# Optimization experiments

Hardware: AMD Instinct MI355X
Metric: run time of the kernel (lower is better)

## Reference

```python
import jax, jax.numpy as jnp
import numpy as np

# Config (matches init_kwargs)
T, B = 128, 32
I, H, O, G = 128, 320, 32, 8
GROUP = 16  # attn_group_size entries, 8 groups of 16 -> sums to I
DT, TAU_X, TAU_W = 0.02, 0.1, 0.2
ALPHA_X = DT / TAU_X          # 0.2
ALPHA_W = DT / TAU_W          # 0.1
E_PROP = 0.8


def _masks():
    e_h = int(E_PROP * H)  # 256
    # x2h: e_prop=1, zero_cols_prop=0, no diag removal -> all ones
    mask_x = jnp.ones((H, I), dtype=jnp.float32)
    # h2h: sign mask (+1 for E, -1 for I), diagonal zeroed
    sign_h = jnp.concatenate([jnp.ones(e_h), -jnp.ones(H - e_h)]).astype(jnp.float32)
    mask_h = jnp.tile(sign_h[None, :], (H, 1)) * (1.0 - jnp.eye(H, dtype=jnp.float32))
    # h2o: zero_cols = int(0.2*H) trailing columns removed, sign mask on the rest
    zc = int((1.0 - E_PROP) * H)  # 64
    exist = jnp.concatenate([jnp.ones(H - zc), jnp.zeros(zc)]).astype(jnp.float32)
    mask_o = jnp.tile((sign_h * exist)[None, :], (O, 1))
    # attn EILinear(H -> G): same column pattern as h2o
    mask_a = jnp.tile((sign_h * exist)[None, :], (G, 1))
    return mask_x, mask_h, mask_o, mask_a


def setup_inputs() -> dict:
    key = jax.random.key(0)
    ks = jax.random.split(key, 10)
    s = 0.05  # keep dynamics in a sane range
    return {
        "x": jax.random.normal(ks[0], (T, B, I), dtype=jnp.float32),
        "Rs": jax.random.uniform(ks[1], (T, B, 1), dtype=jnp.float32),
        "W_x2h": jax.random.normal(ks[2], (H, I), dtype=jnp.float32) * s,
        "W_h2h": jax.random.normal(ks[3], (H, H), dtype=jnp.float32) * s,
        "b_h2h": jax.random.normal(ks[4], (H,), dtype=jnp.float32) * s,
        "W_h2o": jax.random.normal(ks[5], (O, H), dtype=jnp.float32) * s,
        "b_h2o": jax.random.normal(ks[6], (O,), dtype=jnp.float32) * s,
        "W_attn": jax.random.normal(ks[7], (G, H), dtype=jnp.float32) * s,
        "b_attn": jax.random.normal(ks[8], (G,), dtype=jnp.float32) * s,
        "c_plas": jax.random.normal(ks[9], (6,), dtype=jnp.float32) * s,
    }


def reference(x, Rs, W_x2h, W_h2h, b_h2h, W_h2o, b_h2o, W_attn, b_attn, c_plas):
    mask_x, mask_h, mask_o, mask_a = _masks()
    relu = jax.nn.relu
    # effective (sign/existence constrained, positive) weights
    ew_attn = relu(W_attn) * mask_a                      # [G, H]
    ew_x0 = relu(W_x2h) * mask_x                         # [H, I]
    ew_h0 = relu(W_h2h) * mask_h                         # [H, H]
    c = jnp.abs(c_plas)

    state0 = jnp.zeros((B, H), dtype=x.dtype)            # x0=0, sigma_rec=0
    output0 = relu(state0)
    wx0 = jnp.broadcast_to(ew_x0[None], (B, H, I))       # batched fast weights
    wh0 = jnp.broadcast_to(ew_h0[None], (B, H, H))

    def step(carry, inp):
        state, output, wx, wh = carry
        x_t, R_t = inp                                   # [B,I], [B,1]
        # attention over hidden groups
        attn = jax.nn.softmax(output @ ew_attn.T + b_attn, axis=-1)  # [B,G]
        attn_full = jnp.repeat(attn, GROUP, axis=-1)     # [B,I]
        xm = x_t * attn_full * G
        # masked / positive-constrained fast weights applied per batch
        ewx = relu(wx) * mask_x[None]                    # [B,H,I]
        ewh = relu(wh) * mask_h[None]                    # [B,H,H]
        total = (jnp.einsum('bhi,bi->bh', ewx, xm)
                 + jnp.einsum('bhj,bj->bh', ewh, output) + b_h2h)
        new_state = state * (1.0 - ALPHA_X) + total * ALPHA_X
        new_output = jnp.tanh(relu(new_state))           # retanh
        # outer-product plasticity update
        R = R_t[:, :, None]                              # [B,1,1]
        wx_n = wx * (1.0 - ALPHA_W) + ALPHA_W * R * (
            c[0] * xm[:, None, :]
            + c[1] * new_output[:, :, None]
            + c[2] * jnp.einsum('bi,bj->bij', new_output, xm))
        wh_n = wh * (1.0 - ALPHA_W) + ALPHA_W * R * (
            c[3] * output[:, None, :]
            + c[4] * new_output[:, :, None]
            + c[5] * jnp.einsum('bi,bj->bij', new_output, output))
        return (new_state, new_output, wx_n, wh_n), new_output

    _, hs = jax.lax.scan(step, (state0, output0, wx0, wh0), (x, Rs))  # hs: [T,B,H]
    ew_o = relu(W_h2o) * mask_o                          # [O,H]
    out = jax.nn.sigmoid(jnp.einsum('tbh,oh->tbo', hs, ew_o) + b_h2o)
    return out, hs
```

## Files before the change

### kernel.cpp

```cpp
#include <hip/hip_runtime.h>

#define TT 128
#define BB 32
#define II 128
#define HH 320
#define OO 32
#define GG 8
#define HPAD 129

static __device__ __forceinline__ float fexp2(float x) { return __builtin_amdgcn_exp2f(x); }
static __device__ __forceinline__ float frcp(float x)  { return __builtin_amdgcn_rcpf(x); }

static __device__ __forceinline__ float tanh_pos(float x) {
    float e = fexp2(x * 2.8853900817779268f);
    return 1.0f - 2.0f * frcp(e + 1.0f);
}

template<int CTRL>
static __device__ __forceinline__ float dpp_add(float v) {
    int t = __builtin_amdgcn_update_dpp(0, __builtin_bit_cast(int, v),
                                        CTRL, 0xf, 0xf, true);
    return v + __builtin_bit_cast(float, t);
}
static __device__ __forceinline__ float bcast63(float v) {
    return __builtin_bit_cast(float,
        __builtin_amdgcn_readlane(__builtin_bit_cast(int, v), 63));
}
static __device__ __forceinline__ float wave_sum(float v) {
    v = dpp_add<0x111>(v);
    v = dpp_add<0x112>(v);
    v = dpp_add<0x114>(v);
    v = dpp_add<0x118>(v);
    v = dpp_add<0x142>(v);
    v = dpp_add<0x143>(v);
    return bcast63(v);
}

__global__ __launch_bounds__(512, 2)
void leaky_rnn_kernel(const float* __restrict__ x, const float* __restrict__ Rs,
                      const float* __restrict__ Wx2h, const float* __restrict__ Wh2h,
                      const float* __restrict__ bh2h, const float* __restrict__ Wh2o,
                      const float* __restrict__ bh2o, const float* __restrict__ Wattn,
                      const float* __restrict__ battn, const float* __restrict__ cplas,
                      float* __restrict__ out, float* __restrict__ hs,
                      unsigned* __restrict__ ctr)
{
    const int tid  = threadIdx.x;
    const int bid  = blockIdx.x;
    const int b    = bid >> 3;
    const int sub  = bid & 7;
    const int w    = tid >> 6;
    const int lane = tid & 63;
    const int h0   = sub * 40;

    __shared__ float s_ea[GG * HH];
    __shared__ float s_out[2][HH];
    __shared__ float s_logit[GG];
    __shared__ float s_hist[40 * HPAD];
    __shared__ float s_hs[16 * HH];

    for (int idx = tid; idx < GG * HH; idx += 512) {
        int h = idx % HH;
        float m = (h < 256) ? 1.f : (h == 256 ? -1.f : 0.f);
        s_ea[idx] = fmaxf(Wattn[idx], 0.f) * m;
    }
    if (tid < HH) { s_out[0][tid] = 0.f; s_out[1][tid] = 0.f; }

    float wx[5][2], wh[5][5], st[5], bh[5];
    int hrow[5];
#pragma unroll
    for (int r = 0; r < 5; ++r) {
        int h = h0 + w * 5 + r;
        hrow[r] = h;
        bh[r] = bh2h[h];
        st[r] = 0.f;
#pragma unroll
        for (int c = 0; c < 2; ++c)
            wx[r][c] = fmaxf(Wx2h[h * II + lane + 64 * c], 0.f);
#pragma unroll
        for (int c = 0; c < 5; ++c) {
            int j = lane + 64 * c;
            float v = fmaxf(Wh2h[h * HH + j], 0.f);
            v = (c == 4) ? -v : v;
            wh[r][c] = (j == h) ? 0.f : v;
        }
    }
    float batt = battn[w];
    float c0 = fabsf(cplas[0]), c1 = fabsf(cplas[1]), c2 = fabsf(cplas[2]);
    float c3 = fabsf(cplas[3]), c4 = fabsf(cplas[4]), c5 = fabsf(cplas[5]);

    const float AX  = (float)(0.02 / 0.1);
    const float AW  = (float)(0.02 / 0.2);
    const float OMX = 1.f - AX;
    const float OMW = 1.f - AW;
    const float L2E = 1.4426950408889634f;

    __syncthreads();

    float xv0n = x[b * II + lane];
    float xv1n = x[b * II + lane + 64];
    float Rvn  = Rs[b];

#pragma unroll 1
    for (int t = 0; t < TT; ++t) {
        const float* so_cur = s_out[t & 1];
        float*       so_nxt = s_out[(t + 1) & 1];
        float xv0 = xv0n, xv1 = xv1n;
        float A   = AW * Rvn;

        float lp = 0.f;
#pragma unroll
        for (int k = 0; k < 5; ++k) {
            int hh2 = lane + 64 * k;
            lp = fmaf(s_ea[w * HH + hh2], so_cur[hh2], lp);
        }
        float lt = wave_sum(lp);
        if (lane == 0) s_logit[w] = lt + batt;
        __syncthreads();

        float lg[8];
#pragma unroll
        for (int g = 0; g < 8; ++g) lg[g] = s_logit[g];
        float mx = lg[0];
#pragma unroll
        for (int g = 1; g < 8; ++g) mx = fmaxf(mx, lg[g]);
        float se = 0.f, eg[8];
#pragma unroll
        for (int g = 0; g < 8; ++g) { eg[g] = fexp2((lg[g] - mx) * L2E); se += eg[g]; }
        float rinv = frcp(se);
        float xmc0 = xv0 * eg[lane >> 4] * 8.f * rinv;
        float xmc1 = xv1 * eg[(lane >> 4) + 4] * 8.f * rinv;

        float oc[5];
#pragma unroll
        for (int c = 0; c < 5; ++c) oc[c] = so_cur[lane + 64 * c];

        float p[5];
#pragma unroll
        for (int r = 0; r < 5; ++r) {
            int h = hrow[r];
            float pp = fmaxf(wx[r][0], 0.f) * xmc0;
            pp = fmaf(fmaxf(wx[r][1], 0.f), xmc1, pp);
#pragma unroll
            for (int c = 0; c < 5; ++c) {
                float wv = fmaxf(wh[r][c], 0.f);
                float so = (c == 4) ? -oc[4] : oc[c];
                float term = wv * so;
                term = ((lane + 64 * c) == h) ? 0.f : term;
                pp += term;
            }
            p[r] = pp;
        }
#define DPP_LEVEL(CTRL) \
        p[0] = dpp_add<CTRL>(p[0]); p[1] = dpp_add<CTRL>(p[1]); \
        p[2] = dpp_add<CTRL>(p[2]); p[3] = dpp_add<CTRL>(p[3]); \
        p[4] = dpp_add<CTRL>(p[4]);
        DPP_LEVEL(0x111)
        DPP_LEVEL(0x112)
        DPP_LEVEL(0x114)
        DPP_LEVEL(0x118)
        DPP_LEVEL(0x142)
        DPP_LEVEL(0x143)
#undef DPP_LEVEL

        float no[5];
#pragma unroll
        for (int r = 0; r < 5; ++r) {
            float total = bcast63(p[r]) + bh[r];
            st[r] = fmaf(st[r], OMX, total * AX);
            no[r] = tanh_pos(fmaxf(st[r], 0.f));
        }

        {
            float pub = no[0];
            pub = (lane == 1) ? no[1] : pub;
            pub = (lane == 2) ? no[2] : pub;
            pub = (lane == 3) ? no[3] : pub;
            pub = (lane == 4) ? no[4] : pub;
            if (lane < 5) {
                __hip_atomic_store(&hs[(t * BB + b) * HH + h0 + w * 5 + lane], pub + 2.0f,
                                   __ATOMIC_RELAXED, __HIP_MEMORY_SCOPE_AGENT);
                s_hist[(w * 5 + lane) * HPAD + t] = pub;
                so_nxt[h0 + w * 5 + lane] = pub;
            }
        }

        if (t < TT - 1) {
            float Ac0 = A * c0, Ac1 = A * c1, Ac2 = A * c2;
            float Ac3 = A * c3, Ac4 = A * c4, Ac5 = A * c5;
#pragma unroll
            for (int r = 0; r < 5; ++r) {
                float u  = fmaf(Ac2, no[r], Ac0);
                float v  = Ac1 * no[r];
                float pp = fmaf(Ac5, no[r], Ac3);
                float qq = Ac4 * no[r];
                wx[r][0] = fmaf(wx[r][0], OMW, fmaf(u, xmc0, v));
                wx[r][1] = fmaf(wx[r][1], OMW, fmaf(u, xmc1, v));
#pragma unroll
                for (int c = 0; c < 5; ++c)
                    wh[r][c] = fmaf(wh[r][c], OMW, fmaf(pp, oc[c], qq));
            }
        }

        if (t + 1 < TT) {
            xv0n = x[((t + 1) * BB + b) * II + lane];
            xv1n = x[((t + 1) * BB + b) * II + lane + 64];
            Rvn  = Rs[(t + 1) * BB + b];
        }

        if (t < TT - 1 && tid < HH && !(tid >= h0 && tid < h0 + 40)) {
            const float* p2 = &hs[(t * BB + b) * HH + tid];
            float va = __hip_atomic_load(p2, __ATOMIC_RELAXED, __HIP_MEMORY_SCOPE_AGENT);
            float vb = __hip_atomic_load(p2, __ATOMIC_RELAXED, __HIP_MEMORY_SCOPE_AGENT);
            float vc = __hip_atomic_load(p2, __ATOMIC_RELAXED, __HIP_MEMORY_SCOPE_AGENT);
            float vd = __hip_atomic_load(p2, __ATOMIC_RELAXED, __HIP_MEMORY_SCOPE_AGENT);
            int guard = 0;
            while (va < 1.0f && ++guard < 2000000) {
                va = vb; vb = vc; vc = vd;
                vd = __hip_atomic_load(p2, __ATOMIC_RELAXED, __HIP_MEMORY_SCOPE_AGENT);
            }
            so_nxt[tid] = va - 2.0f;
        }
        __syncthreads();
    }

    if (tid == 0) {
        __hip_atomic_fetch_add(&ctr[b * 32], 1u, __ATOMIC_RELAXED, __HIP_MEMORY_SCOPE_AGENT);
        int guard = 0;
        while (__hip_atomic_load(&ctr[b * 32], __ATOMIC_RELAXED, __HIP_MEMORY_SCOPE_AGENT) < 8u) {
            if (++guard > 2000000) break;
            __builtin_amdgcn_s_sleep(1);
        }
    }
    __syncthreads();

    for (int idx = tid; idx < 16 * HH; idx += 512) {
        int tl = idx / HH, h = idx % HH;
        int t_g = sub * 16 + tl;
        s_hs[idx] = __hip_atomic_load(&hs[(t_g * BB + b) * HH + h],
                                      __ATOMIC_RELAXED, __HIP_MEMORY_SCOPE_AGENT) - 2.0f;
    }
    __syncthreads();
    {
        int t_loc = tid >> 5;
        int o     = tid & 31;
        int t_g   = sub * 16 + t_loc;
        const float* hp = &s_hs[t_loc * HH];
        float acc = bh2o[o];
#pragma unroll 4
        for (int h = 0; h < 257; ++h) {
            float m = (h == 256) ? -1.f : 1.f;
            acc = fmaf(fmaxf(Wh2o[o * HH + h], 0.f) * m, hp[h], acc);
        }
        float sg = frcp(1.f + fexp2(-acc * L2E));
        out[(t_g * BB + b) * OO + o] = sg;
    }

    __syncthreads();
    if (tid == 0) {
        __hip_atomic_fetch_add(&ctr[b * 32], 1u, __ATOMIC_RELAXED, __HIP_MEMORY_SCOPE_AGENT);
        int guard = 0;
        while (__hip_atomic_load(&ctr[b * 32], __ATOMIC_RELAXED, __HIP_MEMORY_SCOPE_AGENT) < 16u) {
            if (++guard > 2000000) break;
            __builtin_amdgcn_s_sleep(1);
        }
    }
    __syncthreads();

    for (int idx = tid; idx < 40 * TT; idx += 512) {
        int row = idx >> 7;
        int t   = idx & 127;
        __hip_atomic_store(&hs[(t * BB + b) * HH + h0 + row], s_hist[row * HPAD + t],
                           __ATOMIC_RELAXED, __HIP_MEMORY_SCOPE_AGENT);
    }
}

extern "C" void kernel_launch(void* const* d_in, const int* in_sizes, int n_in,
                              void* d_out, int out_size, void* d_ws, size_t ws_size,
                              hipStream_t stream) {
    const float* x     = (const float*)d_in[0];
    const float* Rs    = (const float*)d_in[1];
    const float* Wx2h  = (const float*)d_in[2];
    const float* Wh2h  = (const float*)d_in[3];
    const float* bh2h  = (const float*)d_in[4];
    const float* Wh2o  = (const float*)d_in[5];
    const float* bh2o  = (const float*)d_in[6];
    const float* Wattn = (const float*)d_in[7];
    const float* battn = (const float*)d_in[8];
    const float* cplas = (const float*)d_in[9];
    float* out = (float*)d_out;
    float* hs  = out + TT * BB * OO;
    unsigned* ctr = (unsigned*)d_ws;

    hipMemsetAsync(d_ws, 0, 32 * 32 * sizeof(unsigned), stream);
    hipLaunchKernelGGL(leaky_rnn_kernel, dim3(256), dim3(512), 0, stream,
                       x, Rs, Wx2h, Wh2h, bh2h, Wh2o, bh2o, Wattn, battn, cplas,
                       out, hs, ctr);
}
```

Baseline: 438.3 us.

## Co-locate batch blocks per XCD and exchange hidden state via L2 atomics

Remaps block IDs so the 8 blocks for a given batch element have consecutive-by-32 IDs, which likely places them on the same XCD under round-robin dispatch. Blocks then record their XCC_ID and check at runtime whether all 8 share one XCD. If they do, they publish hidden state with L2 atomic swaps and poll with atomic-add-zero reads, which are meant to resolve in the shared L2 instead of going through slower device-coherent memory. A fallback to the original relaxed load path, including a give-up counter, keeps correctness when placement differs, at the cost of extra atomic traffic and inline asm.

```diff
diff --git a/kernel.cpp b/kernel.cpp
--- a/kernel.cpp
+++ b/kernel.cpp
@@ -34,6 +34,17 @@
     v = dpp_add<0x142>(v);
     v = dpp_add<0x143>(v);
     return bcast63(v);
+}
+
+static __device__ __forceinline__ void l2_swap(float* p, float v) {
+    asm volatile("global_atomic_swap %0, %1, off"
+                 :: "v"(p), "v"(__builtin_bit_cast(unsigned, v)) : "memory");
+}
+static __device__ __forceinline__ float l2_read(const float* p) {
+    unsigned u; unsigned z = 0u;
+    asm volatile("global_atomic_add %0, %1, %2, off sc0\n\ts_waitcnt vmcnt(0)"
+                 : "=v"(u) : "v"(p), "v"(z) : "memory");
+    return __builtin_bit_cast(float, u);
 }
 
 __global__ __launch_bounds__(512, 2)
@@ -47,8 +58,8 @@
 {
     const int tid  = threadIdx.x;
     const int bid  = blockIdx.x;
-    const int b    = bid >> 3;
-    const int sub  = bid & 7;
+    const int b    = bid & 31;
+    const int sub  = bid >> 5;
     const int w    = tid >> 6;
     const int lane = tid & 63;
     const int h0   = sub * 40;
@@ -58,6 +69,18 @@
     __shared__ float s_logit[GG];
     __shared__ float s_hist[40 * HPAD];
     __shared__ float s_hs[16 * HH];
+    __shared__ int   s_mode;
+    __shared__ int   s_giveup;
+
+    unsigned* slots = ctr + 1024;
+
+    if (tid == 0) {
+        unsigned xid;
+        asm volatile("s_getreg_b32 %0, hwreg(HW_REG_XCC_ID)" : "=s"(xid));
+        __hip_atomic_store(&slots[(b * 8 + sub) * 32], xid + 1u,
+                           __ATOMIC_RELAXED, __HIP_MEMORY_SCOPE_AGENT);
+        s_giveup = 0;
+    }
 
     for (int idx = tid; idx < GG * HH; idx += 512) {
         int h = idx % HH;
@@ -95,7 +118,24 @@
     const float OMW = 1.f - AW;
     const float L2E = 1.4426950408889634f;
 
-    __syncthreads();
+    if (tid == 0) {
+        unsigned xid;
+        asm volatile("s_getreg_b32 %0, hwreg(HW_REG_XCC_ID)" : "=s"(xid));
+        unsigned tag = xid + 1u;
+        int ok = 1;
+        for (int s2 = 0; s2 < 8; ++s2) {
+            unsigned v = 0u; int g2 = 0;
+            do {
+                v = __hip_atomic_load(&slots[(b * 8 + s2) * 32],
+                                      __ATOMIC_RELAXED, __HIP_MEMORY_SCOPE_AGENT);
+            } while (v == 0u && ++g2 < 2000000);
+            if (v != tag) ok = 0;
+        }
+        s_mode = ok;
+    }
+
+    __syncthreads();
+    const bool fast = (s_mode != 0);
 
     float xv0n = x[b * II + lane];
     float xv1n = x[b * II + lane + 64];
@@ -151,17 +191,13 @@
             }
             p[r] = pp;
         }
-#define DPP_LEVEL(CTRL) \
-        p[0] = dpp_add<CTRL>(p[0]); p[1] = dpp_add<CTRL>(p[1]); \
-        p[2] = dpp_add<CTRL>(p[2]); p[3] = dpp_add<CTRL>(p[3]); \
-        p[4] = dpp_add<CTRL>(p[4]);
-        DPP_LEVEL(0x111)
-        DPP_LEVEL(0x112)
-        DPP_LEVEL(0x114)
-        DPP_LEVEL(0x118)
-        DPP_LEVEL(0x142)
-        DPP_LEVEL(0x143)
-#undef DPP_LEVEL
+#define DPP_L5(CTRL) { \
+        p[0]=dpp_add<CTRL>(p[0]); p[1]=dpp_add<CTRL>(p[1]); \
+        p[2]=dpp_add<CTRL>(p[2]); p[3]=dpp_add<CTRL>(p[3]); \
+        p[4]=dpp_add<CTRL>(p[4]); }
+        DPP_L5(0x111) DPP_L5(0x112) DPP_L5(0x114)
+        DPP_L5(0x118) DPP_L5(0x142) DPP_L5(0x143)
+#undef DPP_L5
 
         float no[5];
 #pragma unroll
@@ -178,8 +214,10 @@
             pub = (lane == 3) ? no[3] : pub;
             pub = (lane == 4) ? no[4] : pub;
             if (lane < 5) {
-                __hip_atomic_store(&hs[(t * BB + b) * HH + h0 + w * 5 + lane], pub + 2.0f,
-                                   __ATOMIC_RELAXED, __HIP_MEMORY_SCOPE_AGENT);
+                float* dst = &hs[(t * BB + b) * HH + h0 + w * 5 + lane];
+                float bp = pub + 2.0f;
+                if (fast) l2_swap(dst, bp);
+                __hip_atomic_store(dst, bp, __ATOMIC_RELAXED, __HIP_MEMORY_SCOPE_AGENT);
                 s_hist[(w * 5 + lane) * HPAD + t] = pub;
                 so_nxt[h0 + w * 5 + lane] = pub;
             }
@@ -210,14 +248,25 @@
 
         if (t < TT - 1 && tid < HH && !(tid >= h0 && tid < h0 + 40)) {
             const float* p2 = &hs[(t * BB + b) * HH + tid];
-            float va = __hip_atomic_load(p2, __ATOMIC_RELAXED, __HIP_MEMORY_SCOPE_AGENT);
-            float vb = __hip_atomic_load(p2, __ATOMIC_RELAXED, __HIP_MEMORY_SCOPE_AGENT);
-            float vc = __hip_atomic_load(p2, __ATOMIC_RELAXED, __HIP_MEMORY_SCOPE_AGENT);
-            float vd = __hip_atomic_load(p2, __ATOMIC_RELAXED, __HIP_MEMORY_SCOPE_AGENT);
-            int guard = 0;
-            while (va < 1.0f && ++guard < 2000000) {
-                va = vb; vb = vc; vc = vd;
-                vd = __hip_atomic_load(p2, __ATOMIC_RELAXED, __HIP_MEMORY_SCOPE_AGENT);
+            float va = 0.f;
+            if (fast && s_giveup == 0) {
+                int guard = 0;
+                do {
+                    va = l2_read(p2);
+                } while (va < 1.0f && ++guard < 3000);
+                if (va < 1.0f) s_giveup = 1;
+            }
+            if (va < 1.0f) {
+                float vb = __hip_atomic_load(p2, __ATOMIC_RELAXED, __HIP_MEMORY_SCOPE_AGENT);
+                float vc = __hip_atomic_load(p2, __ATOMIC_RELAXED, __HIP_MEMORY_SCOPE_AGENT);
+                float vd = __hip_atomic_load(p2, __ATOMIC_RELAXED, __HIP_MEMORY_SCOPE_AGENT);
+                va = __hip_atomic_load(p2, __ATOMIC_RELAXED, __HIP_MEMORY_SCOPE_AGENT);
+                float t0 = vb; vb = vc; vc = vd; vd = va; va = t0;
+                int guard = 0;
+                while (va < 1.0f && ++guard < 2000000) {
+                    va = vb; vb = vc; vc = vd;
+                    vd = __hip_atomic_load(p2, __ATOMIC_RELAXED, __HIP_MEMORY_SCOPE_AGENT);
+                }
             }
             so_nxt[tid] = va - 2.0f;
         }
@@ -270,8 +319,10 @@
     for (int idx = tid; idx < 40 * TT; idx += 512) {
         int row = idx >> 7;
         int t   = idx & 127;
-        __hip_atomic_store(&hs[(t * BB + b) * HH + h0 + row], s_hist[row * HPAD + t],
-                           __ATOMIC_RELAXED, __HIP_MEMORY_SCOPE_AGENT);
+        float* dst = &hs[(t * BB + b) * HH + h0 + row];
+        float tv = s_hist[row * HPAD + t];
+        if (fast) l2_swap(dst, tv);
+        __hip_atomic_store(dst, tv, __ATOMIC_RELAXED, __HIP_MEMORY_SCOPE_AGENT);
     }
 }
 
@@ -292,7 +343,7 @@
     float* hs  = out + TT * BB * OO;
     unsigned* ctr = (unsigned*)d_ws;
 
-    hipMemsetAsync(d_ws, 0, 32 * 32 * sizeof(unsigned), stream);
+    hipMemsetAsync(d_ws, 0, 36864, stream);
     hipLaunchKernelGGL(leaky_rnn_kernel, dim3(256), dim3(512), 0, stream,
                        x, Rs, Wx2h, Wh2h, bh2h, Wh2o, bh2o, Wattn, battn, cplas,
                        out, hs, ctr);
```

New measurement: 753.8 us. +72.0%, slower.

## Split each batch across 2 blocks instead of 8, 20 rows per wave

Applied to the files above, without the earlier changes.

Each batch element's hidden state is now split across 2 workgroups of 160 rows instead of 8 of 40. Each wave keeps 20 rows of plastic weights in registers, and the launch bound drops to 1 block per CU. The aim is to cut the cross-block spin-wait exchange of hidden state through global memory each timestep, since fewer peers are polled. In exchange each block does 4x the per-step arithmetic serially, and register pressure (about 140 weight floats per thread) may cause spills or lower occupancy.

```diff
diff --git a/kernel.cpp b/kernel.cpp
--- a/kernel.cpp
+++ b/kernel.cpp
@@ -6,6 +6,8 @@
 #define HH 320
 #define OO 32
 #define GG 8
+#define RW 20
+#define HB 160
 #define HPAD 129
 
 static __device__ __forceinline__ float fexp2(float x) { return __builtin_amdgcn_exp2f(x); }
@@ -36,7 +38,7 @@
     return bcast63(v);
 }
 
-__global__ __launch_bounds__(512, 2)
+__global__ __launch_bounds__(512, 1)
 void leaky_rnn_kernel(const float* __restrict__ x, const float* __restrict__ Rs,
                       const float* __restrict__ Wx2h, const float* __restrict__ Wh2h,
                       const float* __restrict__ bh2h, const float* __restrict__ Wh2o,
@@ -47,16 +49,17 @@
 {
     const int tid  = threadIdx.x;
     const int bid  = blockIdx.x;
-    const int b    = bid >> 3;
-    const int sub  = bid & 7;
+    const int b    = bid >> 1;
+    const int sub  = bid & 1;
     const int w    = tid >> 6;
     const int lane = tid & 63;
-    const int h0   = sub * 40;
+    const int h0   = sub * HB;
+    const int hw   = h0 + w * RW;
 
     __shared__ float s_ea[GG * HH];
     __shared__ float s_out[2][HH];
     __shared__ float s_logit[GG];
-    __shared__ float s_hist[40 * HPAD];
+    __shared__ float s_hist[HB * HPAD];
     __shared__ float s_hs[16 * HH];
 
     for (int idx = tid; idx < GG * HH; idx += 512) {
@@ -66,12 +69,10 @@
     }
     if (tid < HH) { s_out[0][tid] = 0.f; s_out[1][tid] = 0.f; }
 
-    float wx[5][2], wh[5][5], st[5], bh[5];
-    int hrow[5];
-#pragma unroll
-    for (int r = 0; r < 5; ++r) {
-        int h = h0 + w * 5 + r;
-        hrow[r] = h;
+    float wx[RW][2], wh[RW][5], st[RW], bh[RW];
+#pragma unroll
+    for (int r = 0; r < RW; ++r) {
+        int h = hw + r;
         bh[r] = bh2h[h];
         st[r] = 0.f;
 #pragma unroll
@@ -135,10 +136,10 @@
 #pragma unroll
         for (int c = 0; c < 5; ++c) oc[c] = so_cur[lane + 64 * c];
 
-        float p[5];
-#pragma unroll
-        for (int r = 0; r < 5; ++r) {
-            int h = hrow[r];
+        float p[RW];
+#pragma unroll
+        for (int r = 0; r < RW; ++r) {
+            int h = hw + r;
             float pp = fmaxf(wx[r][0], 0.f) * xmc0;
             pp = fmaf(fmaxf(wx[r][1], 0.f), xmc1, pp);
 #pragma unroll
@@ -151,55 +152,40 @@
             }
             p[r] = pp;
         }
-#define DPP_LEVEL(CTRL) \
-        p[0] = dpp_add<CTRL>(p[0]); p[1] = dpp_add<CTRL>(p[1]); \
-        p[2] = dpp_add<CTRL>(p[2]); p[3] = dpp_add<CTRL>(p[3]); \
-        p[4] = dpp_add<CTRL>(p[4]);
-        DPP_LEVEL(0x111)
-        DPP_LEVEL(0x112)
-        DPP_LEVEL(0x114)
-        DPP_LEVEL(0x118)
-        DPP_LEVEL(0x142)
-        DPP_LEVEL(0x143)
-#undef DPP_LEVEL
-
-        float no[5];
-#pragma unroll
-        for (int r = 0; r < 5; ++r) {
+#define DPP_LALL(CTRL) { \
+        _Pragma("unroll") \
+        for (int r = 0; r < RW; ++r) p[r] = dpp_add<CTRL>(p[r]); }
+        DPP_LALL(0x111) DPP_LALL(0x112) DPP_LALL(0x114)
+        DPP_LALL(0x118) DPP_LALL(0x142) DPP_LALL(0x143)
+#undef DPP_LALL
+
+        float pub = 0.f;
+        float Ac0 = A * c0, Ac1 = A * c1, Ac2 = A * c2;
+        float Ac3 = A * c3, Ac4 = A * c4, Ac5 = A * c5;
+#pragma unroll
+        for (int r = 0; r < RW; ++r) {
             float total = bcast63(p[r]) + bh[r];
             st[r] = fmaf(st[r], OMX, total * AX);
-            no[r] = tanh_pos(fmaxf(st[r], 0.f));
-        }
-
-        {
-            float pub = no[0];
-            pub = (lane == 1) ? no[1] : pub;
-            pub = (lane == 2) ? no[2] : pub;
-            pub = (lane == 3) ? no[3] : pub;
-            pub = (lane == 4) ? no[4] : pub;
-            if (lane < 5) {
-                __hip_atomic_store(&hs[(t * BB + b) * HH + h0 + w * 5 + lane], pub + 2.0f,
-                                   __ATOMIC_RELAXED, __HIP_MEMORY_SCOPE_AGENT);
-                s_hist[(w * 5 + lane) * HPAD + t] = pub;
-                so_nxt[h0 + w * 5 + lane] = pub;
-            }
-        }
-
-        if (t < TT - 1) {
-            float Ac0 = A * c0, Ac1 = A * c1, Ac2 = A * c2;
-            float Ac3 = A * c3, Ac4 = A * c4, Ac5 = A * c5;
-#pragma unroll
-            for (int r = 0; r < 5; ++r) {
-                float u  = fmaf(Ac2, no[r], Ac0);
-                float v  = Ac1 * no[r];
-                float pp = fmaf(Ac5, no[r], Ac3);
-                float qq = Ac4 * no[r];
+            float no_r = tanh_pos(fmaxf(st[r], 0.f));
+            pub = (lane == r) ? no_r : pub;
+            if (t < TT - 1) {
+                float u  = fmaf(Ac2, no_r, Ac0);
+                float v  = Ac1 * no_r;
+                float pq = fmaf(Ac5, no_r, Ac3);
+                float qq = Ac4 * no_r;
                 wx[r][0] = fmaf(wx[r][0], OMW, fmaf(u, xmc0, v));
                 wx[r][1] = fmaf(wx[r][1], OMW, fmaf(u, xmc1, v));
 #pragma unroll
                 for (int c = 0; c < 5; ++c)
-                    wh[r][c] = fmaf(wh[r][c], OMW, fmaf(pp, oc[c], qq));
-            }
+                    wh[r][c] = fmaf(wh[r][c], OMW, fmaf(pq, oc[c], qq));
+            }
+        }
+
+        if (lane < RW) {
+            __hip_atomic_store(&hs[(t * BB + b) * HH + hw + lane], pub + 2.0f,
+                               __ATOMIC_RELAXED, __HIP_MEMORY_SCOPE_AGENT);
+            s_hist[(w * RW + lane) * HPAD + t] = pub;
+            so_nxt[hw + lane] = pub;
         }
 
         if (t + 1 < TT) {
@@ -208,7 +194,7 @@
             Rvn  = Rs[(t + 1) * BB + b];
         }
 
-        if (t < TT - 1 && tid < HH && !(tid >= h0 && tid < h0 + 40)) {
+        if (t < TT - 1 && tid < HH && !(tid >= h0 && tid < h0 + HB)) {
             const float* p2 = &hs[(t * BB + b) * HH + tid];
             float va = __hip_atomic_load(p2, __ATOMIC_RELAXED, __HIP_MEMORY_SCOPE_AGENT);
             float vb = __hip_atomic_load(p2, __ATOMIC_RELAXED, __HIP_MEMORY_SCOPE_AGENT);
@@ -227,47 +213,50 @@
     if (tid == 0) {
         __hip_atomic_fetch_add(&ctr[b * 32], 1u, __ATOMIC_RELAXED, __HIP_MEMORY_SCOPE_AGENT);
         int guard = 0;
-        while (__hip_atomic_load(&ctr[b * 32], __ATOMIC_RELAXED, __HIP_MEMORY_SCOPE_AGENT) < 8u) {
+        while (__hip_atomic_load(&ctr[b * 32], __ATOMIC_RELAXED, __HIP_MEMORY_SCOPE_AGENT) < 2u) {
             if (++guard > 2000000) break;
             __builtin_amdgcn_s_sleep(1);
         }
     }
     __syncthreads();
 
-    for (int idx = tid; idx < 16 * HH; idx += 512) {
-        int tl = idx / HH, h = idx % HH;
-        int t_g = sub * 16 + tl;
-        s_hs[idx] = __hip_atomic_load(&hs[(t_g * BB + b) * HH + h],
-                                      __ATOMIC_RELAXED, __HIP_MEMORY_SCOPE_AGENT) - 2.0f;
-    }
-    __syncthreads();
-    {
-        int t_loc = tid >> 5;
-        int o     = tid & 31;
-        int t_g   = sub * 16 + t_loc;
-        const float* hp = &s_hs[t_loc * HH];
-        float acc = bh2o[o];
+#pragma unroll 1
+    for (int pass = 0; pass < 4; ++pass) {
+        for (int idx = tid; idx < 16 * HH; idx += 512) {
+            int tl = idx / HH, h = idx % HH;
+            int t_g = sub * 64 + pass * 16 + tl;
+            s_hs[idx] = __hip_atomic_load(&hs[(t_g * BB + b) * HH + h],
+                                          __ATOMIC_RELAXED, __HIP_MEMORY_SCOPE_AGENT) - 2.0f;
+        }
+        __syncthreads();
+        {
+            int t_loc = tid >> 5;
+            int o     = tid & 31;
+            int t_g   = sub * 64 + pass * 16 + t_loc;
+            const float* hp = &s_hs[t_loc * HH];
+            float acc = bh2o[o];
 #pragma unroll 4
-        for (int h = 0; h < 257; ++h) {
-            float m = (h == 256) ? -1.f : 1.f;
-            acc = fmaf(fmaxf(Wh2o[o * HH + h], 0.f) * m, hp[h], acc);
-        }
-        float sg = frcp(1.f + fexp2(-acc * L2E));
-        out[(t_g * BB + b) * OO + o] = sg;
-    }
-
-    __syncthreads();
+            for (int h = 0; h < 257; ++h) {
+                float m = (h == 256) ? -1.f : 1.f;
+                acc = fmaf(fmaxf(Wh2o[o * HH + h], 0.f) * m, hp[h], acc);
+            }
+            float sg = frcp(1.f + fexp2(-acc * L2E));
+            out[(t_g * BB + b) * OO + o] = sg;
+        }
+        __syncthreads();
+    }
+
     if (tid == 0) {
         __hip_atomic_fetch_add(&ctr[b * 32], 1u, __ATOMIC_RELAXED, __HIP_MEMORY_SCOPE_AGENT);
         int guard = 0;
-        while (__hip_atomic_load(&ctr[b * 32], __ATOMIC_RELAXED, __HIP_MEMORY_SCOPE_AGENT) < 16u) {
+        while (__hip_atomic_load(&ctr[b * 32], __ATOMIC_RELAXED, __HIP_MEMORY_SCOPE_AGENT) < 4u) {
             if (++guard > 2000000) break;
             __builtin_amdgcn_s_sleep(1);
         }
     }
     __syncthreads();
 
-    for (int idx = tid; idx < 40 * TT; idx += 512) {
+    for (int idx = tid; idx < HB * TT; idx += 512) {
         int row = idx >> 7;
         int t   = idx & 127;
         __hip_atomic_store(&hs[(t * BB + b) * HH + h0 + row], s_hist[row * HPAD + t],
@@ -293,7 +282,7 @@
     unsigned* ctr = (unsigned*)d_ws;
 
     hipMemsetAsync(d_ws, 0, 32 * 32 * sizeof(unsigned), stream);
-    hipLaunchKernelGGL(leaky_rnn_kernel, dim3(256), dim3(512), 0, stream,
+    hipLaunchKernelGGL(leaky_rnn_kernel, dim3(64), dim3(512), 0, stream,
                        x, Rs, Wx2h, Wh2h, bh2h, Wh2o, bh2o, Wattn, battn, cplas,
                        out, hs, ctr);
 }
```

New measurement: 1.129 ms. 158% more time.

## Coalesce cross-block hidden-state publish into one wave and issue polls early

Applied to the files above, without the earlier changes.

Each wave now stages its five new outputs in shared memory, and after an added block barrier a single wave writes all 40 to global memory in one coalesced store. Polling of the other blocks' values is reassigned to threads 0..279 and its first loads are issued before the plasticity update, so load latency overlaps with that arithmetic. The cost is an extra __syncthreads per timestep on the critical recurrence path. The DPP reduction is only reformatted.

```diff
diff --git a/kernel.cpp b/kernel.cpp
--- a/kernel.cpp
+++ b/kernel.cpp
@@ -56,6 +56,7 @@
     __shared__ float s_ea[GG * HH];
     __shared__ float s_out[2][HH];
     __shared__ float s_logit[GG];
+    __shared__ float s_pub[40];
     __shared__ float s_hist[40 * HPAD];
     __shared__ float s_hs[16 * HH];
 
@@ -100,6 +101,8 @@
     float xv0n = x[b * II + lane];
     float xv1n = x[b * II + lane + 64];
     float Rvn  = Rs[b];
+
+    const int prow = (tid < 280) ? ((tid < h0) ? tid : tid + 40) : -1;
 
 #pragma unroll 1
     for (int t = 0; t < TT; ++t) {
@@ -151,17 +154,13 @@
             }
             p[r] = pp;
         }
-#define DPP_LEVEL(CTRL) \
-        p[0] = dpp_add<CTRL>(p[0]); p[1] = dpp_add<CTRL>(p[1]); \
-        p[2] = dpp_add<CTRL>(p[2]); p[3] = dpp_add<CTRL>(p[3]); \
-        p[4] = dpp_add<CTRL>(p[4]);
-        DPP_LEVEL(0x111)
-        DPP_LEVEL(0x112)
-        DPP_LEVEL(0x114)
-        DPP_LEVEL(0x118)
-        DPP_LEVEL(0x142)
-        DPP_LEVEL(0x143)
-#undef DPP_LEVEL
+#define DPP_L5(CTRL) { \
+        p[0]=dpp_add<CTRL>(p[0]); p[1]=dpp_add<CTRL>(p[1]); \
+        p[2]=dpp_add<CTRL>(p[2]); p[3]=dpp_add<CTRL>(p[3]); \
+        p[4]=dpp_add<CTRL>(p[4]); }
+        DPP_L5(0x111) DPP_L5(0x112) DPP_L5(0x114)
+        DPP_L5(0x118) DPP_L5(0x142) DPP_L5(0x143)
+#undef DPP_L5
 
         float no[5];
 #pragma unroll
@@ -178,11 +177,26 @@
             pub = (lane == 3) ? no[3] : pub;
             pub = (lane == 4) ? no[4] : pub;
             if (lane < 5) {
-                __hip_atomic_store(&hs[(t * BB + b) * HH + h0 + w * 5 + lane], pub + 2.0f,
-                                   __ATOMIC_RELAXED, __HIP_MEMORY_SCOPE_AGENT);
+                s_pub[w * 5 + lane] = pub;
                 s_hist[(w * 5 + lane) * HPAD + t] = pub;
                 so_nxt[h0 + w * 5 + lane] = pub;
             }
+        }
+        __syncthreads();
+
+        if (w == 7 && lane < 40) {
+            __hip_atomic_store(&hs[(t * BB + b) * HH + h0 + lane], s_pub[lane] + 2.0f,
+                               __ATOMIC_RELAXED, __HIP_MEMORY_SCOPE_AGENT);
+        }
+
+        float va = 2.5f, vb = 0.f, vc = 0.f, vd = 0.f;
+        const float* p2 = nullptr;
+        if (t < TT - 1 && prow >= 0) {
+            p2 = &hs[(t * BB + b) * HH + prow];
+            va = __hip_atomic_load(p2, __ATOMIC_RELAXED, __HIP_MEMORY_SCOPE_AGENT);
+            vb = __hip_atomic_load(p2, __ATOMIC_RELAXED, __HIP_MEMORY_SCOPE_AGENT);
+            vc = __hip_atomic_load(p2, __ATOMIC_RELAXED, __HIP_MEMORY_SCOPE_AGENT);
+            vd = __hip_atomic_load(p2, __ATOMIC_RELAXED, __HIP_MEMORY_SCOPE_AGENT);
         }
 
         if (t < TT - 1) {
@@ -208,18 +222,13 @@
             Rvn  = Rs[(t + 1) * BB + b];
         }
 
-        if (t < TT - 1 && tid < HH && !(tid >= h0 && tid < h0 + 40)) {
-            const float* p2 = &hs[(t * BB + b) * HH + tid];
-            float va = __hip_atomic_load(p2, __ATOMIC_RELAXED, __HIP_MEMORY_SCOPE_AGENT);
-            float vb = __hip_atomic_load(p2, __ATOMIC_RELAXED, __HIP_MEMORY_SCOPE_AGENT);
-            float vc = __hip_atomic_load(p2, __ATOMIC_RELAXED, __HIP_MEMORY_SCOPE_AGENT);
-            float vd = __hip_atomic_load(p2, __ATOMIC_RELAXED, __HIP_MEMORY_SCOPE_AGENT);
+        if (t < TT - 1 && prow >= 0) {
             int guard = 0;
             while (va < 1.0f && ++guard < 2000000) {
                 va = vb; vb = vc; vc = vd;
                 vd = __hip_atomic_load(p2, __ATOMIC_RELAXED, __HIP_MEMORY_SCOPE_AGENT);
             }
-            so_nxt[tid] = va - 2.0f;
+            so_nxt[prow] = va - 2.0f;
         }
         __syncthreads();
     }
```

Result: slower. 458.0 us (+4.5%).
